# Optimization experiments

Hardware: AMD Instinct MI355X
Metric: run time of the kernel (lower is better)

## Reference

```python
import jax, jax.numpy as jnp
import numpy as np

BS, S, F, D, M = 64, 1024, 3, 128, 4


def _lin(k, fan_in, fan_out):
    return jax.random.normal(k, (fan_in, fan_out), jnp.float32) * 0.02


def setup_inputs() -> dict:
    key = jax.random.key(0)
    ks = jax.random.split(key, 24)
    inp = {
        "x": jax.random.normal(ks[0], (BS, S, F), jnp.float32),
        "n": jax.random.randint(ks[1], (BS, 1), 1, S + 1, jnp.int32),
        "query": jnp.zeros((BS, M, D), jnp.float32),
        # SetFunc: H (3072->1024->128) then G (128->64->2)
        "sh1_w": _lin(ks[2], S * F, 1024), "sh1_b": jnp.zeros((1024,), jnp.float32),
        "sh2_w": _lin(ks[3], 1024, D),     "sh2_b": jnp.zeros((D,), jnp.float32),
        "sg1_w": _lin(ks[4], D, 64),       "sg1_b": jnp.zeros((64,), jnp.float32),
        "sg2_w": _lin(ks[5], 64, 2),       "sg2_b": jnp.zeros((2,), jnp.float32),
        # 4 attention heads: projection weight [5,D] and per-head H params (stacked)
        "attn_w": jax.random.normal(ks[6], (M, 5, D), jnp.float32) * 0.02,
        "ah1_w": jax.random.normal(ks[7], (M, S * F, 1024), jnp.float32) * 0.02,
        "ah1_b": jnp.zeros((M, 1024), jnp.float32),
        "ah2_w": jax.random.normal(ks[8], (M, 1024, D), jnp.float32) * 0.02,
        "ah2_b": jnp.zeros((M, D), jnp.float32),
        # head MLP: 512->256->64->1
        "f1_w": _lin(ks[9], D * M, 256), "f1_b": jnp.zeros((256,), jnp.float32),
        "f2_w": _lin(ks[10], 256, 64),   "f2_b": jnp.zeros((64,), jnp.float32),
        "f3_w": _lin(ks[11], 64, 1),     "f3_b": jnp.zeros((1,), jnp.float32),
    }
    return inp


def reference(x, n, query, sh1_w, sh1_b, sh2_w, sh2_b, sg1_w, sg1_b, sg2_w, sg2_b,
              attn_w, ah1_w, ah1_b, ah2_w, ah2_b, f1_w, f1_b, f2_w, f2_b, f3_w, f3_b):
    bs = x.shape[0]
    xf = x.reshape(bs, -1)                       # (bs, 3072)
    nf = n.astype(jnp.float32)                    # (bs, 1)

    # SetFunc: e = G(H(x) / n) -> f_S (bs, 2)
    e = jax.nn.relu(jax.nn.relu(xf @ sh1_w + sh1_b) @ sh2_w + sh2_b) / nf
    f_S = jax.nn.relu(jax.nn.relu(e @ sg1_w + sg1_b) @ sg2_w + sg2_b)

    # matrix[:, :, 0:2] = f_S broadcast, matrix[:, :, 2:5] = x
    matrix = jnp.concatenate(
        [jnp.broadcast_to(f_S[:, None, :], (bs, S, 2)), x], axis=2)  # (bs, S, 5)

    q0 = query[:, 0, :]                           # (bs, D)
    pos = jnp.arange(S)
    mask = pos[None, :] >= n                      # (bs, S) ragged length mask
    inv_sqrt_d = 1.0 / jnp.sqrt(jnp.float32(D))

    def head(w5, hw1, hb1, hw2, hb2):
        key_ = jnp.einsum('bsf,fd->bsd', matrix, w5)                 # (bs, S, D)
        e_ji = jnp.einsum('bsd,bd->bs', key_, q0) * inv_sqrt_d        # (bs, S)
        e_ji = jnp.where(mask, -1000.0, e_ji)
        a = jax.nn.softmax(e_ji, axis=1)                              # (bs, S)
        h_s = jax.nn.relu(jax.nn.relu(xf @ hw1 + hb1) @ hw2 + hb2)    # (bs, D)
        # original: r[k] = sum_s a[k,s] * h_s[k]  ==  h_s * sum_s a
        return h_s * jnp.sum(a, axis=1, keepdims=True)

    r = jax.vmap(head)(attn_w, ah1_w, ah1_b, ah2_w, ah2_b)            # (M, bs, D)
    r = jnp.transpose(r, (1, 0, 2)).reshape(bs, -1)                   # (bs, M*D)

    y = jax.nn.relu(r @ f1_w + f1_b)   # dropout is identity at eval
    y = jax.nn.relu(y @ f2_w + f2_b)
    return jax.nn.sigmoid(y @ f3_w + f3_b)        # (bs, 1)
```

## Files before the change

### kernel.cpp

```cpp
#include <hip/hip_runtime.h>
#include <hip/hip_bf16.h>


#define K1   3072
#define N1   1024
#define KSPL 4
#define KRNG 768
#define BK   32
#define NIT  24
#define BN   32

typedef short bf16x8 __attribute__((ext_vector_type(8)));
typedef float f32x4  __attribute__((ext_vector_type(4)));
typedef unsigned short ushort4v __attribute__((ext_vector_type(4)));

__device__ __forceinline__ unsigned short f2b(float f) {
  unsigned int u = __float_as_uint(f);
  unsigned int r = (u + 0x7FFFu + ((u >> 16) & 1u)) >> 16;
  return (unsigned short)r;
}
__device__ __forceinline__ float relu(float v) { return v > 0.f ? v : 0.f; }

__global__ void k_convert_x(const float* __restrict__ x, unsigned short* __restrict__ A) {
  int i = (blockIdx.x * 256 + threadIdx.x) * 4;
  float4 v = *reinterpret_cast<const float4*>(x + i);
  ushort4v o;
  o.x = f2b(v.x); o.y = f2b(v.y); o.z = f2b(v.z); o.w = f2b(v.w);
  *reinterpret_cast<ushort4v*>(A + i) = o;
}

__device__ __forceinline__ int bchunk(int c, int q) {
  return c * 4 + (q ^ (c & 3) ^ ((c >> 2) & 3));
}

__global__ __launch_bounds__(256, 2) void k_gemm1(
    const unsigned short* __restrict__ A,
    const float* __restrict__ W,
    float* __restrict__ part)
{
  __shared__ __align__(16) unsigned short Bt[BN * BK];

  const int nt = blockIdx.x, ks = blockIdx.y, h = blockIdx.z;
  const int tid = threadIdx.x;
  const float* Wg = W + (size_t)h * K1 * N1 + nt * BN;
  const int kbase = ks * KRNG;

  const int skr = tid >> 3;
  const int sc4 = (tid & 7) * 4;
  const int w = tid >> 6, lane = tid & 63, lr = lane & 15, lkg = lane >> 4;

  const unsigned short* Ap = A + (size_t)(16 * w + lr) * K1 + kbase + lkg * 8;

  f32x4 acc0 = {0.f, 0.f, 0.f, 0.f}, acc1 = {0.f, 0.f, 0.f, 0.f};

  float4 bpre = *reinterpret_cast<const float4*>(Wg + (size_t)(kbase + skr) * N1 + sc4);
  bf16x8 apre = *reinterpret_cast<const bf16x8*>(Ap);

  for (int it = 0; it < NIT; ++it) {
    {
      const int q = skr >> 3, klo = skr & 7;
      Bt[bchunk(sc4 + 0, q) * 8 + klo] = f2b(bpre.x);
      Bt[bchunk(sc4 + 1, q) * 8 + klo] = f2b(bpre.y);
      Bt[bchunk(sc4 + 2, q) * 8 + klo] = f2b(bpre.z);
      Bt[bchunk(sc4 + 3, q) * 8 + klo] = f2b(bpre.w);
    }
    __syncthreads();
    bf16x8 af  = apre;
    bf16x8 bf0 = *reinterpret_cast<const bf16x8*>(&Bt[bchunk(lr,      lkg) * 8]);
    bf16x8 bf1 = *reinterpret_cast<const bf16x8*>(&Bt[bchunk(16 + lr, lkg) * 8]);
    if (it + 1 < NIT) {
      const int kn = kbase + (it + 1) * BK;
      bpre = *reinterpret_cast<const float4*>(Wg + (size_t)(kn + skr) * N1 + sc4);
      apre = *reinterpret_cast<const bf16x8*>(Ap + (it + 1) * BK);
    }
    acc0 = __builtin_amdgcn_mfma_f32_16x16x32_bf16(af, bf0, acc0, 0, 0, 0);
    acc1 = __builtin_amdgcn_mfma_f32_16x16x32_bf16(af, bf1, acc1, 0, 0, 0);
    __syncthreads();
  }

  float* P = part + ((size_t)ks * 4 + h) * (64 * N1)
                  + (size_t)(16 * w + lkg * 4) * N1 + nt * BN + lr;
#pragma unroll
  for (int i = 0; i < 4; ++i) {
    P[(size_t)i * N1]      = acc0[i];
    P[(size_t)i * N1 + 16] = acc1[i];
  }
}

__global__ void k_reduce_relu(const float* __restrict__ part,
                              const float* __restrict__ b1,
                              float* __restrict__ h1)
{
  int i = (blockIdx.x * 256 + threadIdx.x) * 4;
  float4 s0 = *reinterpret_cast<const float4*>(part + i);
  float4 s1 = *reinterpret_cast<const float4*>(part + i + 262144);
  float4 s2 = *reinterpret_cast<const float4*>(part + i + 524288);
  float4 s3 = *reinterpret_cast<const float4*>(part + i + 786432);
  float4 b  = *reinterpret_cast<const float4*>(b1 + (i >> 16) * 1024 + (i & 1023));
  float4 o;
  o.x = relu(s0.x + s1.x + s2.x + s3.x + b.x);
  o.y = relu(s0.y + s1.y + s2.y + s3.y + b.y);
  o.z = relu(s0.z + s1.z + s2.z + s3.z + b.z);
  o.w = relu(s0.w + s1.w + s2.w + s3.w + b.w);
  *reinterpret_cast<float4*>(h1 + i) = o;
}

__global__ __launch_bounds__(512) void k_gemm2(
    const float* __restrict__ h1,
    const float* __restrict__ W2,
    float* __restrict__ r)
{
  const int b = blockIdx.x, h = blockIdx.y;
  const int t = threadIdx.x;
  const int d = t & 127, ksl = t >> 7;
  const float* hr = h1 + ((size_t)h * 64 + b) * 1024 + ksl * 256;
  const float* Wp = W2 + (size_t)h * 1024 * 128 + (size_t)ksl * 256 * 128 + d;
  float a0 = 0.f, a1 = 0.f, a2 = 0.f, a3 = 0.f;
#pragma unroll 4
  for (int k = 0; k < 256; k += 4) {
    a0 += hr[k + 0] * Wp[(size_t)(k + 0) * 128];
    a1 += hr[k + 1] * Wp[(size_t)(k + 1) * 128];
    a2 += hr[k + 2] * Wp[(size_t)(k + 2) * 128];
    a3 += hr[k + 3] * Wp[(size_t)(k + 3) * 128];
  }
  __shared__ float red[4][128];
  red[ksl][d] = a0 + a1 + a2 + a3;
  __syncthreads();
  if (t < 128) {
    float s = red[0][t] + red[1][t] + red[2][t] + red[3][t];
    r[(size_t)b * 512 + h * 128 + t] = s;
  }
}

__global__ __launch_bounds__(512) void k_final(
    const float* __restrict__ r,
    const float* __restrict__ b2,
    const float* __restrict__ f1w, const float* __restrict__ f1b,
    const float* __restrict__ f2w, const float* __restrict__ f2b,
    const float* __restrict__ f3w, const float* __restrict__ f3b,
    float* __restrict__ out)
{
  const int b = blockIdx.x, t = threadIdx.x;
  __shared__ float rr[512];
  __shared__ float y1p[2][256];
  __shared__ float y1[256];
  __shared__ float y2p[4][64];
  __shared__ float y2[64];

  rr[t] = relu(r[(size_t)b * 512 + t] + b2[t]);
  __syncthreads();

  {
    const int j = t & 255, kh = t >> 8;
    const float* W = f1w + (size_t)kh * 256 * 256 + j;
    const float* rv = rr + kh * 256;
    float a0 = 0.f, a1 = 0.f, a2 = 0.f, a3 = 0.f;
#pragma unroll 4
    for (int k = 0; k < 256; k += 4) {
      a0 += rv[k + 0] * W[(size_t)(k + 0) * 256];
      a1 += rv[k + 1] * W[(size_t)(k + 1) * 256];
      a2 += rv[k + 2] * W[(size_t)(k + 2) * 256];
      a3 += rv[k + 3] * W[(size_t)(k + 3) * 256];
    }
    y1p[kh][j] = a0 + a1 + a2 + a3;
  }
  __syncthreads();
  if (t < 256) y1[t] = relu(y1p[0][t] + y1p[1][t] + f1b[t]);
  __syncthreads();

  if (t < 256) {
    const int j = t & 63, kh = t >> 6;
    const float* W = f2w + (size_t)kh * 64 * 64 + j;
    const float* yv = y1 + kh * 64;
    float a = 0.f;
#pragma unroll 4
    for (int k = 0; k < 64; ++k) a += yv[k] * W[(size_t)k * 64];
    y2p[kh][j] = a;
  }
  __syncthreads();
  if (t < 64) y2[t] = relu(y2p[0][t] + y2p[1][t] + y2p[2][t] + y2p[3][t] + f2b[t]);
  __syncthreads();

  if (t == 0) {
    float s = f3b[0];
#pragma unroll 8
    for (int k = 0; k < 64; ++k) s += y2[k] * f3w[k];
    out[b] = 1.f / (1.f + expf(-s));
  }
}

extern "C" void kernel_launch(void* const* d_in, const int* in_sizes, int n_in,
                              void* d_out, int out_size, void* d_ws, size_t ws_size,
                              hipStream_t stream) {
  (void)in_sizes; (void)n_in; (void)out_size; (void)ws_size;
  const float* x     = (const float*)d_in[0];
  const float* ah1_w = (const float*)d_in[12];
  const float* ah1_b = (const float*)d_in[13];
  const float* ah2_w = (const float*)d_in[14];
  const float* ah2_b = (const float*)d_in[15];
  const float* f1w   = (const float*)d_in[16];
  const float* f1b   = (const float*)d_in[17];
  const float* f2w   = (const float*)d_in[18];
  const float* f2b   = (const float*)d_in[19];
  const float* f3w   = (const float*)d_in[20];
  const float* f3b   = (const float*)d_in[21];
  float* out = (float*)d_out;

  char* ws = (char*)d_ws;
  unsigned short* A = (unsigned short*)ws;
  float* part = (float*)(ws + 524288);
  float* h1   = (float*)(ws + 524288 + 4194304);
  float* r    = (float*)(ws + 524288 + 4194304 + 1048576);

  k_convert_x<<<192, 256, 0, stream>>>(x, A);
  k_gemm1<<<dim3(32, KSPL, 4), 256, 0, stream>>>(A, ah1_w, part);
  k_reduce_relu<<<256, 256, 0, stream>>>(part, ah1_b, h1);
  k_gemm2<<<dim3(64, 4), 512, 0, stream>>>(h1, ah2_w, r);
  k_final<<<64, 512, 0, stream>>>(r, ah2_b, f1w, f1b, f2w, f2b, f3w, f3b, out);
}
```

Before: 168.8 us.

## Fuse x conversion into GEMM1, fuse reduce into GEMM2, bf16 head weights

The separate x-to-bf16 kernel is removed, and GEMM1 now converts fp32 x in registers with a two-deep software prefetch. The split-K reduce plus ReLU is folded into a retiled GEMM2 (8 batch rows x 128-k slice per block), which writes per-slice partials that k_final sums. GEMM2 blocks also convert f1w and f2w to bf16 for k_final's MLP, which halves those weight reads but adds rounding error. Overall this cuts two launches and the h1 round trip through memory.

```diff
diff --git a/kernel.cpp b/kernel.cpp
--- a/kernel.cpp
+++ b/kernel.cpp
@@ -16,25 +16,19 @@
 
 __device__ __forceinline__ unsigned short f2b(float f) {
   unsigned int u = __float_as_uint(f);
-  unsigned int r = (u + 0x7FFFu + ((u >> 16) & 1u)) >> 16;
-  return (unsigned short)r;
+  return (unsigned short)((u + 0x7FFFu + ((u >> 16) & 1u)) >> 16);
+}
+__device__ __forceinline__ float b2f(unsigned short b) {
+  return __uint_as_float(((unsigned int)b) << 16);
 }
 __device__ __forceinline__ float relu(float v) { return v > 0.f ? v : 0.f; }
-
-__global__ void k_convert_x(const float* __restrict__ x, unsigned short* __restrict__ A) {
-  int i = (blockIdx.x * 256 + threadIdx.x) * 4;
-  float4 v = *reinterpret_cast<const float4*>(x + i);
-  ushort4v o;
-  o.x = f2b(v.x); o.y = f2b(v.y); o.z = f2b(v.z); o.w = f2b(v.w);
-  *reinterpret_cast<ushort4v*>(A + i) = o;
-}
 
 __device__ __forceinline__ int bchunk(int c, int q) {
   return c * 4 + (q ^ (c & 3) ^ ((c >> 2) & 3));
 }
 
 __global__ __launch_bounds__(256, 2) void k_gemm1(
-    const unsigned short* __restrict__ A,
+    const float* __restrict__ x,
     const float* __restrict__ W,
     float* __restrict__ part)
 {
@@ -42,41 +36,54 @@
 
   const int nt = blockIdx.x, ks = blockIdx.y, h = blockIdx.z;
   const int tid = threadIdx.x;
-  const float* Wg = W + (size_t)h * K1 * N1 + nt * BN;
   const int kbase = ks * KRNG;
-
   const int skr = tid >> 3;
   const int sc4 = (tid & 7) * 4;
   const int w = tid >> 6, lane = tid & 63, lr = lane & 15, lkg = lane >> 4;
 
-  const unsigned short* Ap = A + (size_t)(16 * w + lr) * K1 + kbase + lkg * 8;
+  const float* Wp = W + (size_t)h * K1 * N1 + (size_t)(kbase + skr) * N1
+                      + nt * BN + sc4;
+  const float* Ap = x + (size_t)(16 * w + lr) * K1 + kbase + lkg * 8;
 
   f32x4 acc0 = {0.f, 0.f, 0.f, 0.f}, acc1 = {0.f, 0.f, 0.f, 0.f};
 
-  float4 bpre = *reinterpret_cast<const float4*>(Wg + (size_t)(kbase + skr) * N1 + sc4);
-  bf16x8 apre = *reinterpret_cast<const bf16x8*>(Ap);
-
-  for (int it = 0; it < NIT; ++it) {
-    {
-      const int q = skr >> 3, klo = skr & 7;
-      Bt[bchunk(sc4 + 0, q) * 8 + klo] = f2b(bpre.x);
-      Bt[bchunk(sc4 + 1, q) * 8 + klo] = f2b(bpre.y);
-      Bt[bchunk(sc4 + 2, q) * 8 + klo] = f2b(bpre.z);
-      Bt[bchunk(sc4 + 3, q) * 8 + klo] = f2b(bpre.w);
-    }
-    __syncthreads();
-    bf16x8 af  = apre;
-    bf16x8 bf0 = *reinterpret_cast<const bf16x8*>(&Bt[bchunk(lr,      lkg) * 8]);
-    bf16x8 bf1 = *reinterpret_cast<const bf16x8*>(&Bt[bchunk(16 + lr, lkg) * 8]);
-    if (it + 1 < NIT) {
-      const int kn = kbase + (it + 1) * BK;
-      bpre = *reinterpret_cast<const float4*>(Wg + (size_t)(kn + skr) * N1 + sc4);
-      apre = *reinterpret_cast<const bf16x8*>(Ap + (it + 1) * BK);
-    }
-    acc0 = __builtin_amdgcn_mfma_f32_16x16x32_bf16(af, bf0, acc0, 0, 0, 0);
-    acc1 = __builtin_amdgcn_mfma_f32_16x16x32_bf16(af, bf1, acc1, 0, 0, 0);
-    __syncthreads();
-  }
+  float4 bwA = *(const float4*)(Wp);
+  float4 axA = *(const float4*)(Ap);
+  float4 ayA = *(const float4*)(Ap + 4);
+  float4 bwB = *(const float4*)(Wp + (size_t)BK * N1);
+  float4 axB = *(const float4*)(Ap + BK);
+  float4 ayB = *(const float4*)(Ap + BK + 4);
+
+#define G1_BODY(BW, AX, AY, IT)                                            \
+  {                                                                        \
+    const int q_ = skr >> 3, klo_ = skr & 7;                               \
+    Bt[bchunk(sc4 + 0, q_) * 8 + klo_] = f2b(BW.x);                        \
+    Bt[bchunk(sc4 + 1, q_) * 8 + klo_] = f2b(BW.y);                        \
+    Bt[bchunk(sc4 + 2, q_) * 8 + klo_] = f2b(BW.z);                        \
+    Bt[bchunk(sc4 + 3, q_) * 8 + klo_] = f2b(BW.w);                        \
+    __syncthreads();                                                       \
+    bf16x8 af;                                                             \
+    af[0] = (short)f2b(AX.x); af[1] = (short)f2b(AX.y);                    \
+    af[2] = (short)f2b(AX.z); af[3] = (short)f2b(AX.w);                    \
+    af[4] = (short)f2b(AY.x); af[5] = (short)f2b(AY.y);                    \
+    af[6] = (short)f2b(AY.z); af[7] = (short)f2b(AY.w);                    \
+    bf16x8 bf0 = *(const bf16x8*)&Bt[bchunk(lr,      lkg) * 8];            \
+    bf16x8 bf1 = *(const bf16x8*)&Bt[bchunk(16 + lr, lkg) * 8];            \
+    if ((IT) + 2 < NIT) {                                                  \
+      BW = *(const float4*)(Wp + (size_t)((IT) + 2) * BK * N1);            \
+      AX = *(const float4*)(Ap + ((IT) + 2) * BK);                         \
+      AY = *(const float4*)(Ap + ((IT) + 2) * BK + 4);                     \
+    }                                                                      \
+    acc0 = __builtin_amdgcn_mfma_f32_16x16x32_bf16(af, bf0, acc0, 0, 0, 0);\
+    acc1 = __builtin_amdgcn_mfma_f32_16x16x32_bf16(af, bf1, acc1, 0, 0, 0);\
+    __syncthreads();                                                       \
+  }
+
+  for (int it = 0; it < NIT; it += 2) {
+    G1_BODY(bwA, axA, ayA, it);
+    G1_BODY(bwB, axB, ayB, it + 1);
+  }
+#undef G1_BODY
 
   float* P = part + ((size_t)ks * 4 + h) * (64 * N1)
                   + (size_t)(16 * w + lkg * 4) * N1 + nt * BN + lr;
@@ -87,56 +94,78 @@
   }
 }
 
-__global__ void k_reduce_relu(const float* __restrict__ part,
-                              const float* __restrict__ b1,
-                              float* __restrict__ h1)
+__global__ __launch_bounds__(256) void k_gemm2(
+    const float* __restrict__ part,
+    const float* __restrict__ b1,
+    const float* __restrict__ W2,
+    const float* __restrict__ f1w,
+    const float* __restrict__ f2w,
+    float* __restrict__ rpart,
+    unsigned short* __restrict__ f1wb,
+    unsigned short* __restrict__ f2wb)
 {
-  int i = (blockIdx.x * 256 + threadIdx.x) * 4;
-  float4 s0 = *reinterpret_cast<const float4*>(part + i);
-  float4 s1 = *reinterpret_cast<const float4*>(part + i + 262144);
-  float4 s2 = *reinterpret_cast<const float4*>(part + i + 524288);
-  float4 s3 = *reinterpret_cast<const float4*>(part + i + 786432);
-  float4 b  = *reinterpret_cast<const float4*>(b1 + (i >> 16) * 1024 + (i & 1023));
-  float4 o;
-  o.x = relu(s0.x + s1.x + s2.x + s3.x + b.x);
-  o.y = relu(s0.y + s1.y + s2.y + s3.y + b.y);
-  o.z = relu(s0.z + s1.z + s2.z + s3.z + b.z);
-  o.w = relu(s0.w + s1.w + s2.w + s3.w + b.w);
-  *reinterpret_cast<float4*>(h1 + i) = o;
-}
-
-__global__ __launch_bounds__(512) void k_gemm2(
-    const float* __restrict__ h1,
-    const float* __restrict__ W2,
-    float* __restrict__ r)
-{
-  const int b = blockIdx.x, h = blockIdx.y;
+  __shared__ float hl[8][128];
+  const int bg = blockIdx.x, kslc = blockIdx.y, h = blockIdx.z;
   const int t = threadIdx.x;
-  const int d = t & 127, ksl = t >> 7;
-  const float* hr = h1 + ((size_t)h * 64 + b) * 1024 + ksl * 256;
-  const float* Wp = W2 + (size_t)h * 1024 * 128 + (size_t)ksl * 256 * 128 + d;
+
+  {
+    const int bl = t >> 5, kq = t & 31;
+    const int brow = bg * 8 + bl, kg = kslc * 128 + kq * 4;
+    float4 s = {0.f, 0.f, 0.f, 0.f};
+#pragma unroll
+    for (int ksp = 0; ksp < 4; ++ksp) {
+      float4 p = *(const float4*)&part[(((size_t)ksp * 4 + h) * 64 + brow) * 1024 + kg];
+      s.x += p.x; s.y += p.y; s.z += p.z; s.w += p.w;
+    }
+    float4 bb = *(const float4*)&b1[h * 1024 + kg];
+    float4 o;
+    o.x = relu(s.x + bb.x); o.y = relu(s.y + bb.y);
+    o.z = relu(s.z + bb.z); o.w = relu(s.w + bb.w);
+    *(float4*)&hl[bl][kq * 4] = o;
+  }
+  __syncthreads();
+
+  const int bl = t >> 5, dg = t & 31;
+  const float* Wp = W2 + (size_t)h * 131072 + (size_t)(kslc * 128) * 128 + dg * 4;
   float a0 = 0.f, a1 = 0.f, a2 = 0.f, a3 = 0.f;
 #pragma unroll 4
-  for (int k = 0; k < 256; k += 4) {
-    a0 += hr[k + 0] * Wp[(size_t)(k + 0) * 128];
-    a1 += hr[k + 1] * Wp[(size_t)(k + 1) * 128];
-    a2 += hr[k + 2] * Wp[(size_t)(k + 2) * 128];
-    a3 += hr[k + 3] * Wp[(size_t)(k + 3) * 128];
-  }
-  __shared__ float red[4][128];
-  red[ksl][d] = a0 + a1 + a2 + a3;
-  __syncthreads();
-  if (t < 128) {
-    float s = red[0][t] + red[1][t] + red[2][t] + red[3][t];
-    r[(size_t)b * 512 + h * 128 + t] = s;
+  for (int kk4 = 0; kk4 < 32; ++kk4) {
+    float4 h4 = *(const float4*)&hl[bl][kk4 * 4];
+    float4 w0 = *(const float4*)(Wp + (size_t)(kk4 * 4 + 0) * 128);
+    float4 w1 = *(const float4*)(Wp + (size_t)(kk4 * 4 + 1) * 128);
+    float4 w2 = *(const float4*)(Wp + (size_t)(kk4 * 4 + 2) * 128);
+    float4 w3 = *(const float4*)(Wp + (size_t)(kk4 * 4 + 3) * 128);
+    a0 += h4.x * w0.x; a1 += h4.x * w0.y; a2 += h4.x * w0.z; a3 += h4.x * w0.w;
+    a0 += h4.y * w1.x; a1 += h4.y * w1.y; a2 += h4.y * w1.z; a3 += h4.y * w1.w;
+    a0 += h4.z * w2.x; a1 += h4.z * w2.y; a2 += h4.z * w2.z; a3 += h4.z * w2.w;
+    a0 += h4.w * w3.x; a1 += h4.w * w3.y; a2 += h4.w * w3.z; a3 += h4.w * w3.w;
+  }
+  {
+    float4 o = {a0, a1, a2, a3};
+    *(float4*)(rpart + ((size_t)kslc * 64 + (bg * 8 + bl)) * 512 + h * 128 + dg * 4) = o;
+  }
+
+  const int cid = bg * 8 + kslc;
+  if (h == 0) {
+    const int base = (cid * 256 + t) * 8;
+    float4 v0 = *(const float4*)(f1w + base);
+    float4 v1 = *(const float4*)(f1w + base + 4);
+    ushort4v o0, o1;
+    o0.x = f2b(v0.x); o0.y = f2b(v0.y); o0.z = f2b(v0.z); o0.w = f2b(v0.w);
+    o1.x = f2b(v1.x); o1.y = f2b(v1.y); o1.z = f2b(v1.z); o1.w = f2b(v1.w);
+    *(ushort4v*)(f1wb + base) = o0;
+    *(ushort4v*)(f1wb + base + 4) = o1;
+  } else if (h == 1) {
+    const int idx = cid * 256 + t;
+    f2wb[idx] = f2b(f2w[idx]);
   }
 }
 
 __global__ __launch_bounds__(512) void k_final(
-    const float* __restrict__ r,
+    const float* __restrict__ rpart,
     const float* __restrict__ b2,
-    const float* __restrict__ f1w, const float* __restrict__ f1b,
-    const float* __restrict__ f2w, const float* __restrict__ f2b,
+    const unsigned short* __restrict__ f1wb, const float* __restrict__ f1b,
+    const unsigned short* __restrict__ f2wb, const float* __restrict__ f2bv,
     const float* __restrict__ f3w, const float* __restrict__ f3b,
     float* __restrict__ out)
 {
@@ -147,20 +176,25 @@
   __shared__ float y2p[4][64];
   __shared__ float y2[64];
 
-  rr[t] = relu(r[(size_t)b * 512 + t] + b2[t]);
+  {
+    float s = 0.f;
+#pragma unroll
+    for (int sl = 0; sl < 8; ++sl) s += rpart[((size_t)sl * 64 + b) * 512 + t];
+    rr[t] = relu(s + b2[t]);
+  }
   __syncthreads();
 
   {
     const int j = t & 255, kh = t >> 8;
-    const float* W = f1w + (size_t)kh * 256 * 256 + j;
+    const unsigned short* W = f1wb + kh * 256 * 256 + j;
     const float* rv = rr + kh * 256;
     float a0 = 0.f, a1 = 0.f, a2 = 0.f, a3 = 0.f;
 #pragma unroll 4
     for (int k = 0; k < 256; k += 4) {
-      a0 += rv[k + 0] * W[(size_t)(k + 0) * 256];
-      a1 += rv[k + 1] * W[(size_t)(k + 1) * 256];
-      a2 += rv[k + 2] * W[(size_t)(k + 2) * 256];
-      a3 += rv[k + 3] * W[(size_t)(k + 3) * 256];
+      a0 += rv[k + 0] * b2f(W[(size_t)(k + 0) * 256]);
+      a1 += rv[k + 1] * b2f(W[(size_t)(k + 1) * 256]);
+      a2 += rv[k + 2] * b2f(W[(size_t)(k + 2) * 256]);
+      a3 += rv[k + 3] * b2f(W[(size_t)(k + 3) * 256]);
     }
     y1p[kh][j] = a0 + a1 + a2 + a3;
   }
@@ -170,15 +204,15 @@
 
   if (t < 256) {
     const int j = t & 63, kh = t >> 6;
-    const float* W = f2w + (size_t)kh * 64 * 64 + j;
+    const unsigned short* W = f2wb + kh * 64 * 64 + j;
     const float* yv = y1 + kh * 64;
     float a = 0.f;
 #pragma unroll 4
-    for (int k = 0; k < 64; ++k) a += yv[k] * W[(size_t)k * 64];
+    for (int k = 0; k < 64; ++k) a += yv[k] * b2f(W[(size_t)k * 64]);
     y2p[kh][j] = a;
   }
   __syncthreads();
-  if (t < 64) y2[t] = relu(y2p[0][t] + y2p[1][t] + y2p[2][t] + y2p[3][t] + f2b[t]);
+  if (t < 64) y2[t] = relu(y2p[0][t] + y2p[1][t] + y2p[2][t] + y2p[3][t] + f2bv[t]);
   __syncthreads();
 
   if (t == 0) {
@@ -201,20 +235,20 @@
   const float* f1w   = (const float*)d_in[16];
   const float* f1b   = (const float*)d_in[17];
   const float* f2w   = (const float*)d_in[18];
-  const float* f2b   = (const float*)d_in[19];
+  const float* f2b_  = (const float*)d_in[19];
   const float* f3w   = (const float*)d_in[20];
   const float* f3b   = (const float*)d_in[21];
   float* out = (float*)d_out;
 
   char* ws = (char*)d_ws;
-  unsigned short* A = (unsigned short*)ws;
-  float* part = (float*)(ws + 524288);
-  float* h1   = (float*)(ws + 524288 + 4194304);
-  float* r    = (float*)(ws + 524288 + 4194304 + 1048576);
-
-  k_convert_x<<<192, 256, 0, stream>>>(x, A);
-  k_gemm1<<<dim3(32, KSPL, 4), 256, 0, stream>>>(A, ah1_w, part);
-  k_reduce_relu<<<256, 256, 0, stream>>>(part, ah1_b, h1);
-  k_gemm2<<<dim3(64, 4), 512, 0, stream>>>(h1, ah2_w, r);
-  k_final<<<64, 512, 0, stream>>>(r, ah2_b, f1w, f1b, f2w, f2b, f3w, f3b, out);
-}
+  float* part = (float*)ws;
+  float* rpart = (float*)(ws + 4194304);
+  unsigned short* f1wb = (unsigned short*)(ws + 5242880);
+  unsigned short* f2wb = (unsigned short*)(ws + 5505024);
+
+  k_gemm1<<<dim3(32, KSPL, 4), 256, 0, stream>>>(x, ah1_w, part);
+  k_gemm2<<<dim3(8, 8, 4), 256, 0, stream>>>(part, ah1_b, ah2_w, f1w, f2w,
+                                             rpart, f1wb, f2wb);
+  k_final<<<64, 512, 0, stream>>>(rpart, ah2_b, f1wb, f1b, f2wb, f2b_,
+                                  f3w, f3b, out);
+}
```

Result: slower. 172.6 us (+2.2%).
